# Kernel optimization log

Measured on AMD Instinct MI355X. Metric: run time of the kernel, lower is better.

Reference implementation:

```python
import jax, jax.numpy as jnp
import numpy as np

N_NODES = 100000
N_EDGES = 1600000
NFEAT = 256
NHID = 64
NHEADS = 8
NCLASS = 97
ALPHA = 0.2  # leaky relu slope
EPS = 1e-16  # guard against isolated rows (pyGAT divides by e_rowsum directly)


def _sp_gat_layer(x, Wk, ak, src, dst, n_nodes, alpha, concat):
    """One SpGraphAttentionLayer (eval mode, dropout off).
    x: [N, f_in], Wk: [f_in, f_out], ak: [2*f_out].
    edge e_ij = exp(-leakyrelu(a . [h_i || h_j])), out[i] = sum_j e_ij h_j / sum_j e_ij.
    """
    h = x @ Wk                          # [N, f_out]
    f_out = Wk.shape[1]
    s_src = h @ ak[:f_out]              # [N] = a1 . h_i
    s_dst = h @ ak[f_out:]              # [N] = a2 . h_j
    e = jnp.exp(-jax.nn.leaky_relu(s_src[src] + s_dst[dst], negative_slope=alpha))  # [E]
    rowsum = jax.ops.segment_sum(e, src, num_segments=n_nodes)                       # [N]
    num = jax.ops.segment_sum(e[:, None] * h[dst], src, num_segments=n_nodes)        # [N, f_out]
    h_prime = num / (rowsum[:, None] + EPS)
    return jax.nn.elu(h_prime) if concat else h_prime


def setup_inputs() -> dict:
    key = jax.random.key(0)
    ks = jax.random.split(key, 6)
    gain = 1.414  # xavier gain used by pyGAT
    features = jax.random.normal(ks[0], (N_NODES, NFEAT), dtype=jnp.float32)
    edge_index = jax.random.randint(ks[1], (2, N_EDGES), 0, N_NODES, dtype=jnp.int64)
    W = jax.random.normal(ks[2], (NHEADS, NFEAT, NHID), dtype=jnp.float32) * (gain * np.sqrt(2.0 / (NFEAT + NHID)))
    a = jax.random.normal(ks[3], (NHEADS, 2 * NHID), dtype=jnp.float32) * (gain * np.sqrt(2.0 / (1 + 2 * NHID)))
    W_out = jax.random.normal(ks[4], (NHEADS * NHID, NCLASS), dtype=jnp.float32) * (gain * np.sqrt(2.0 / (NHEADS * NHID + NCLASS)))
    a_out = jax.random.normal(ks[5], (2 * NCLASS,), dtype=jnp.float32) * (gain * np.sqrt(2.0 / (1 + 2 * NCLASS)))
    return {"features": features, "W": W, "a": a, "W_out": W_out, "a_out": a_out, "edge_index": edge_index}


def reference(features, W, a, W_out, a_out, edge_index):
    src, dst = edge_index[0], edge_index[1]
    n = features.shape[0]
    # multi-head hidden layer, concat heads (loop over small fixed head count to bound memory)
    heads = [
        _sp_gat_layer(features, W[k], a[k], src, dst, n, ALPHA, concat=True)
        for k in range(W.shape[0])
    ]
    x = jnp.concatenate(heads, axis=1)  # [N, nheads*nhid]
    # output attention layer (concat=False), then elu + log_softmax as in SpGAT.forward
    x = _sp_gat_layer(x, W_out, a_out, src, dst, n, ALPHA, concat=False)
    return jax.nn.log_softmax(jax.nn.elu(x), axis=1)
```

## Files before the change

kernel.cpp:

```cpp
#include <hip/hip_runtime.h>
#include <hip/hip_bf16.h>
#include <stdint.h>

typedef __attribute__((ext_vector_type(8))) short short8;
typedef __attribute__((ext_vector_type(4))) float floatx4;
typedef uint32_t u32;

#define N_NODES 100000
#define N_EDGES 1600000
#define ALPHA_SLOPE 0.2f
#define EPS_F 1e-16f

static __device__ __forceinline__ float bf2f(ushort h) {
    u32 u = ((u32)h) << 16;
    return __builtin_bit_cast(float, u);
}
static __device__ __forceinline__ ushort f2bf(float f) {
    u32 u = __builtin_bit_cast(u32, f);
    u32 r = (u + 0x7fffu + ((u >> 16) & 1u)) >> 16;
    return (ushort)r;
}
static __device__ __forceinline__ float edge_e(float s) {
    float lr = s > 0.f ? s : ALPHA_SLOPE * s;
    return __expf(-lr);
}

__global__ __launch_bounds__(256) void conv_feat(
    const float* __restrict__ in, ushort* __restrict__ out, int n4)
{
    int i = blockIdx.x * 256 + threadIdx.x;
    if (i < n4) {
        float4 v = ((const float4*)in)[i];
        ushort4 o;
        o.x = f2bf(v.x); o.y = f2bf(v.y); o.z = f2bf(v.z); o.w = f2bf(v.w);
        ((ushort4*)out)[i] = o;
    }
}

__global__ __launch_bounds__(256) void pretranspose(
    const float* __restrict__ W, const float* __restrict__ Wout,
    const float* __restrict__ a, const float* __restrict__ aout,
    ushort* __restrict__ Bp1, ushort* __restrict__ Bp2,
    float* __restrict__ acol1, float* __restrict__ acol2)
{
    int idx = blockIdx.x * 256 + threadIdx.x;
    if (idx < 256 * 512) {
        int k = idx >> 9, n = idx & 511;
        int head = n >> 6, c = n & 63;
        Bp1[((size_t)(k >> 3) * 512 + n) * 8 + (k & 7)] = f2bf(W[head * 16384 + k * 64 + c]);
    }
    if (idx < 512 * 128) {
        int k = idx >> 7, n = idx & 127;
        ushort v = (n < 97) ? f2bf(Wout[k * 97 + n]) : (ushort)0;
        Bp2[((size_t)(k >> 3) * 128 + n) * 8 + (k & 7)] = v;
    }
    if (idx < 512) {
        int head = idx >> 6, c = idx & 63;
        acol1[idx * 2]     = a[head * 128 + c];
        acol1[idx * 2 + 1] = a[head * 128 + 64 + c];
    }
    if (idx < 128) {
        acol2[idx * 2]     = (idx < 97) ? aout[idx] : 0.f;
        acol2[idx * 2 + 1] = (idx < 97) ? aout[97 + idx] : 0.f;
    }
}

__global__ __launch_bounds__(256) void gemm_mfma(
    const ushort* __restrict__ A, const ushort* __restrict__ Bp,
    ushort* __restrict__ C, const float* __restrict__ acol,
    float* __restrict__ ssrc_arr, float* __restrict__ sdst_arr,
    int sstride, int M, int K, int NP)
{
    __shared__ __align__(16) ushort Ald[4 * 128 * 8];
    const int tid = threadIdx.x;
    const int lane = tid & 63;
    const int wave = tid >> 6;
    const int wr = wave >> 1, wc = wave & 1;
    const int row0 = blockIdx.x * 128;
    const int col0 = blockIdx.y * 128;
    const int quad = lane >> 4;
    const int l16 = lane & 15;

    floatx4 acc[4][4] = {};

    for (int k0 = 0; k0 < K; k0 += 32) {
        __syncthreads();
#pragma unroll
        for (int i = 0; i < 2; ++i) {
            int q = i * 256 + tid;
            int r = q >> 2, kq = q & 3;
            int row = row0 + r;
            if (row >= M) row = M - 1;
            const uint4* src = (const uint4*)(A + (size_t)row * K + k0 + kq * 8);
            *(uint4*)(&Ald[((kq * 128 + r) * 8)]) = *src;
        }
        __syncthreads();

        short8 bfrag[4];
        int kqg = (k0 >> 3) + quad;
#pragma unroll
        for (int nt = 0; nt < 4; ++nt) {
            int col = col0 + wc * 64 + nt * 16 + l16;
            bfrag[nt] = *(const short8*)(Bp + ((size_t)kqg * NP + col) * 8);
        }
#pragma unroll
        for (int mt = 0; mt < 4; ++mt) {
            int r = wr * 64 + mt * 16 + l16;
            short8 afrag = *(const short8*)(&Ald[(quad * 128 + r) * 8]);
#pragma unroll
            for (int nt = 0; nt < 4; ++nt) {
                acc[mt][nt] = __builtin_amdgcn_mfma_f32_16x16x32_bf16(afrag, bfrag[nt], acc[mt][nt], 0, 0, 0);
            }
        }
    }

#pragma unroll
    for (int mt = 0; mt < 4; ++mt) {
#pragma unroll
        for (int rr = 0; rr < 4; ++rr) {
            int row = row0 + wr * 64 + mt * 16 + quad * 4 + rr;
            if (row < M) {
#pragma unroll
                for (int nt = 0; nt < 4; ++nt) {
                    int col = col0 + wc * 64 + nt * 16 + l16;
                    C[(size_t)row * NP + col] = f2bf(acc[mt][nt][rr]);
                }
            }
        }
    }

    float av1[4], av2[4];
#pragma unroll
    for (int nt = 0; nt < 4; ++nt) {
        int col = col0 + wc * 64 + nt * 16 + l16;
        av1[nt] = acol[col * 2];
        av2[nt] = acol[col * 2 + 1];
    }
    int g = (col0 + wc * 64) >> 6;
    int goff = (sstride > 1) ? g : 0;
#pragma unroll
    for (int mt = 0; mt < 4; ++mt) {
#pragma unroll
        for (int rr = 0; rr < 4; ++rr) {
            float p1 = 0.f, p2 = 0.f;
#pragma unroll
            for (int nt = 0; nt < 4; ++nt) {
                p1 = fmaf(acc[mt][nt][rr], av1[nt], p1);
                p2 = fmaf(acc[mt][nt][rr], av2[nt], p2);
            }
#pragma unroll
            for (int o = 1; o < 16; o <<= 1) {
                p1 += __shfl_xor(p1, o);
                p2 += __shfl_xor(p2, o);
            }
            int row = row0 + wr * 64 + mt * 16 + quad * 4 + rr;
            if (l16 == 0 && row < M) {
                atomicAdd(&ssrc_arr[(size_t)row * sstride + goff], p1);
                atomicAdd(&sdst_arr[(size_t)row * sstride + goff], p2);
            }
        }
    }
}

__global__ __launch_bounds__(256) void hist(const int* __restrict__ ei, int* __restrict__ cnt, int E) {
    int e = blockIdx.x * 256 + threadIdx.x;
    if (e < E) atomicAdd(&cnt[ei[e]], 1);
}

__global__ __launch_bounds__(256) void scan_partial(const int* __restrict__ cnt, int* __restrict__ bsum, int N) {
    int idx = blockIdx.x * 256 + threadIdx.x;
    int v = (idx < N) ? cnt[idx] : 0;
#pragma unroll
    for (int o = 32; o; o >>= 1) v += __shfl_xor(v, o);
    __shared__ int ws[4];
    if ((threadIdx.x & 63) == 0) ws[threadIdx.x >> 6] = v;
    __syncthreads();
    if (threadIdx.x == 0) bsum[blockIdx.x] = ws[0] + ws[1] + ws[2] + ws[3];
}

__global__ __launch_bounds__(512) void scan_block(int* __restrict__ bsum, int nb) {
    __shared__ int s[512];
    int t = threadIdx.x;
    int v = (t < nb) ? bsum[t] : 0;
    s[t] = v;
    __syncthreads();
    for (int o = 1; o < 512; o <<= 1) {
        int u = (t >= o) ? s[t - o] : 0;
        __syncthreads();
        s[t] += u;
        __syncthreads();
    }
    if (t < nb) bsum[t] = s[t] - v;
}

__global__ __launch_bounds__(256) void scan_final(
    const int* __restrict__ cnt, const int* __restrict__ bsum,
    int* __restrict__ row_ptr, int N, int E)
{
    int b = blockIdx.x, t = threadIdx.x;
    int idx = b * 256 + t;
    int v = (idx < N) ? cnt[idx] : 0;
    __shared__ int s[256];
    s[t] = v;
    __syncthreads();
    for (int o = 1; o < 256; o <<= 1) {
        int u = (t >= o) ? s[t - o] : 0;
        __syncthreads();
        s[t] += u;
        __syncthreads();
    }
    if (idx < N) row_ptr[idx] = bsum[b] + s[t] - v;
    if (idx == 0) row_ptr[N] = E;
}

__global__ __launch_bounds__(256) void fill_csr(
    const int* __restrict__ ei, const int* __restrict__ row_ptr,
    int* __restrict__ cur, int* __restrict__ col_idx, int* __restrict__ srow, int E)
{
    int e = blockIdx.x * 256 + threadIdx.x;
    if (e >= E) return;
    int s = ei[e];
    int d = ei[E + e];
    int p = atomicAdd(&cur[s], 1);
    int slot = row_ptr[s] + p;
    col_idx[slot] = d;
    srow[slot] = s;
}

__global__ __launch_bounds__(256) void ea1(
    const int* __restrict__ row_ptr, const int* __restrict__ col_idx,
    const ushort* __restrict__ h_all, const float* __restrict__ ssrc1,
    const float* __restrict__ sdst1, ushort* __restrict__ x1)
{
    int w = blockIdx.x * 4 + (threadIdx.x >> 6);
    int l = threadIdx.x & 63;
    int hl = l >> 3;
    int start = row_ptr[w], end = row_ptr[w + 1];
    float si = ssrc1[(size_t)w * 8 + hl];
    float acc[8] = {};
    float re = 0.f;
    int j = start;
    for (; j + 4 <= end; j += 4) {
        int d0 = col_idx[j], d1 = col_idx[j + 1], d2 = col_idx[j + 2], d3 = col_idx[j + 3];
        float e0 = edge_e(si + sdst1[(size_t)d0 * 8 + hl]);
        float e1 = edge_e(si + sdst1[(size_t)d1 * 8 + hl]);
        float e2 = edge_e(si + sdst1[(size_t)d2 * 8 + hl]);
        float e3 = edge_e(si + sdst1[(size_t)d3 * 8 + hl]);
        short8 v0 = *(const short8*)(h_all + (size_t)d0 * 512 + l * 8);
        short8 v1 = *(const short8*)(h_all + (size_t)d1 * 512 + l * 8);
        short8 v2 = *(const short8*)(h_all + (size_t)d2 * 512 + l * 8);
        short8 v3 = *(const short8*)(h_all + (size_t)d3 * 512 + l * 8);
        re += (e0 + e1) + (e2 + e3);
#pragma unroll
        for (int q = 0; q < 8; ++q) {
            float t0 = fmaf(e0, bf2f((ushort)v0[q]), e1 * bf2f((ushort)v1[q]));
            float t1 = fmaf(e2, bf2f((ushort)v2[q]), e3 * bf2f((ushort)v3[q]));
            acc[q] += t0 + t1;
        }
    }
    for (; j < end; ++j) {
        int d = col_idx[j];
        float e = edge_e(si + sdst1[(size_t)d * 8 + hl]);
        short8 hv = *(const short8*)(h_all + (size_t)d * 512 + l * 8);
        re += e;
#pragma unroll
        for (int q = 0; q < 8; ++q)
            acc[q] = fmaf(e, bf2f((ushort)hv[q]), acc[q]);
    }
    float inv = 1.f / (re + EPS_F);
    short8 o;
#pragma unroll
    for (int q = 0; q < 8; ++q) {
        float p = acc[q] * inv;
        p = p > 0.f ? p : expm1f(p);
        o[q] = (short)f2bf(p);
    }
    __builtin_nontemporal_store(o, (short8*)(x1 + (size_t)w * 512 + l * 8));
}

__global__ __launch_bounds__(256) void ea2(
    const int* __restrict__ row_ptr, const int* __restrict__ col_idx,
    const ushort* __restrict__ h2p, const float* __restrict__ s2src,
    const float* __restrict__ s2dst, float* __restrict__ out)
{
    int w = blockIdx.x * 4 + (threadIdx.x >> 6);
    int l = threadIdx.x & 63;
    int start = row_ptr[w], end = row_ptr[w + 1];
    float si = s2src[w];
    float a0 = 0.f, a1 = 0.f, re = 0.f;
    int j = start;
    for (; j + 4 <= end; j += 4) {
        int d0 = col_idx[j], d1 = col_idx[j + 1], d2 = col_idx[j + 2], d3 = col_idx[j + 3];
        float e0 = edge_e(si + s2dst[d0]);
        float e1 = edge_e(si + s2dst[d1]);
        float e2 = edge_e(si + s2dst[d2]);
        float e3 = edge_e(si + s2dst[d3]);
        u32 h0 = *(const u32*)(h2p + (size_t)d0 * 128 + 2 * l);
        u32 h1 = *(const u32*)(h2p + (size_t)d1 * 128 + 2 * l);
        u32 h2 = *(const u32*)(h2p + (size_t)d2 * 128 + 2 * l);
        u32 h3 = *(const u32*)(h2p + (size_t)d3 * 128 + 2 * l);
        re += (e0 + e1) + (e2 + e3);
        a0 += fmaf(e0, bf2f((ushort)(h0 & 0xffffu)), e1 * bf2f((ushort)(h1 & 0xffffu)))
            + fmaf(e2, bf2f((ushort)(h2 & 0xffffu)), e3 * bf2f((ushort)(h3 & 0xffffu)));
        a1 += fmaf(e0, bf2f((ushort)(h0 >> 16)), e1 * bf2f((ushort)(h1 >> 16)))
            + fmaf(e2, bf2f((ushort)(h2 >> 16)), e3 * bf2f((ushort)(h3 >> 16)));
    }
    for (; j < end; ++j) {
        int d = col_idx[j];
        float e = edge_e(si + s2dst[d]);
        u32 hv = *(const u32*)(h2p + (size_t)d * 128 + 2 * l);
        re += e;
        a0 = fmaf(e, bf2f((ushort)(hv & 0xffffu)), a0);
        a1 = fmaf(e, bf2f((ushort)(hv >> 16)), a1);
    }
    float inv = 1.f / (re + EPS_F);
    float v0 = a0 * inv, v1 = a1 * inv;
    v0 = v0 > 0.f ? v0 : expm1f(v0);
    v1 = v1 > 0.f ? v1 : expm1f(v1);
    int c0 = 2 * l, c1 = 2 * l + 1;
    bool val0 = c0 < 97, val1 = c1 < 97;
    float m = fmaxf(val0 ? v0 : -1e30f, val1 ? v1 : -1e30f);
#pragma unroll
    for (int o = 32; o; o >>= 1) m = fmaxf(m, __shfl_xor(m, o));
    float ex = (val0 ? __expf(v0 - m) : 0.f) + (val1 ? __expf(v1 - m) : 0.f);
#pragma unroll
    for (int o = 32; o; o >>= 1) ex += __shfl_xor(ex, o);
    float lt = m + logf(ex);
    if (val0) __builtin_nontemporal_store(v0 - lt, out + (size_t)w * 97 + c0);
    if (val1) __builtin_nontemporal_store(v1 - lt, out + (size_t)w * 97 + c1);
}

extern "C" void kernel_launch(void* const* d_in, const int* in_sizes, int n_in,
                              void* d_out, int out_size, void* d_ws, size_t ws_size,
                              hipStream_t stream)
{
    const float* feat = (const float*)d_in[0];
    const float* W    = (const float*)d_in[1];
    const float* a    = (const float*)d_in[2];
    const float* Wout = (const float*)d_in[3];
    const float* aout = (const float*)d_in[4];
    const int*   ei   = (const int*)d_in[5];
    float* out = (float*)d_out;

    const int N = N_NODES, E = N_EDGES;
    const int NB = (N + 255) / 256;

    char* base = (char*)d_ws;
    ushort* h_all = (ushort*)(base);
    ushort* x1    = (ushort*)(base + 102400000);
    ushort* featb = (ushort*)(base + 204800000);
    ushort* h2p   = (ushort*)(base + 204800000);
    char* tail = base + 256000000;
    float* ssrc1   = (float*)(tail + 0);
    float* sdst1   = (float*)(tail + 3200000);
    float* s2src   = (float*)(tail + 6400000);
    float* s2dst   = (float*)(tail + 6800000);
    int*   row_ptr = (int*)(tail + 7200000);
    int*   cnt     = (int*)(tail + 7600128);
    int*   col_idx = (int*)(tail + 8000128);
    int*   bsum    = (int*)(tail + 14400128);
    ushort* Bp1    = (ushort*)(tail + 14401920);
    ushort* Bp2    = (ushort*)(tail + 14664064);
    float* acol1   = (float*)(tail + 14795136);
    float* acol2   = (float*)(tail + 14799232);
    int*   srow    = (int*)(tail + 14800256);

    hipMemsetAsync(cnt, 0, (size_t)N * 4, stream);
    hipMemsetAsync(ssrc1, 0, (size_t)7200000, stream);
    conv_feat<<<(N * 256 / 4 + 255) / 256, 256, 0, stream>>>(feat, featb, N * 256 / 4);
    pretranspose<<<512, 256, 0, stream>>>(W, Wout, a, aout, Bp1, Bp2, acol1, acol2);

    gemm_mfma<<<dim3(782, 4), 256, 0, stream>>>(featb, Bp1, h_all, acol1, ssrc1, sdst1, 8, N, 256, 512);

    hist<<<(E + 255) / 256, 256, 0, stream>>>(ei, cnt, E);
    scan_partial<<<NB, 256, 0, stream>>>(cnt, bsum, N);
    scan_block<<<1, 512, 0, stream>>>(bsum, NB);
    scan_final<<<NB, 256, 0, stream>>>(cnt, bsum, row_ptr, N, E);
    hipMemsetAsync(cnt, 0, (size_t)N * 4, stream);
    fill_csr<<<(E + 255) / 256, 256, 0, stream>>>(ei, row_ptr, cnt, col_idx, srow, E);

    ea1<<<N / 4, 256, 0, stream>>>(row_ptr, col_idx, h_all, ssrc1, sdst1, x1);

    gemm_mfma<<<dim3(782, 1), 256, 0, stream>>>(x1, Bp2, h2p, acol2, s2src, s2dst, 1, N, 512, 128);
    ea2<<<N / 4, 256, 0, stream>>>(row_ptr, col_idx, h2p, s2src, s2dst, out);
}
```

Measured before the change: 865.5 us.

## Fuse prep kernels, deepen GEMM K-tile with swizzled LDS, narrow ea2 rows

Merges feature conversion, weight pre-transpose and the edge histogram into one prep kernel, and folds the memsets into a single contiguous clear with a separate cursor array. The GEMM now stages 64-wide K tiles into XOR-swizzled LDS and swaps grid axes so column blocks of the same row tile launch together. fill_csr stops writing the unused srow array, and ea2 handles a row with 32 lanes loading 4 bf16 values each. The aim is fewer launches, fewer LDS barriers and bank conflicts, and less wasted memory traffic. The risks are a larger LDS footprint and less parallelism per row in ea2.

```diff
diff --git a/kernel.cpp b/kernel.cpp
--- a/kernel.cpp
+++ b/kernel.cpp
@@ -25,43 +25,44 @@
     return __expf(-lr);
 }
 
-__global__ __launch_bounds__(256) void conv_feat(
-    const float* __restrict__ in, ushort* __restrict__ out, int n4)
-{
-    int i = blockIdx.x * 256 + threadIdx.x;
-    if (i < n4) {
-        float4 v = ((const float4*)in)[i];
+__global__ __launch_bounds__(256) void prep(
+    const float* __restrict__ feat, const float* __restrict__ W,
+    const float* __restrict__ Wout, const float* __restrict__ a,
+    const float* __restrict__ aout, const int* __restrict__ ei,
+    ushort* __restrict__ featb, ushort* __restrict__ Bp1, ushort* __restrict__ Bp2,
+    float* __restrict__ acol1, float* __restrict__ acol2, int* __restrict__ cnt)
+{
+    int b = blockIdx.x;
+    if (b < 25000) {
+        int i = b * 256 + threadIdx.x;
+        float4 v = ((const float4*)feat)[i];
         ushort4 o;
         o.x = f2bf(v.x); o.y = f2bf(v.y); o.z = f2bf(v.z); o.w = f2bf(v.w);
-        ((ushort4*)out)[i] = o;
-    }
-}
-
-__global__ __launch_bounds__(256) void pretranspose(
-    const float* __restrict__ W, const float* __restrict__ Wout,
-    const float* __restrict__ a, const float* __restrict__ aout,
-    ushort* __restrict__ Bp1, ushort* __restrict__ Bp2,
-    float* __restrict__ acol1, float* __restrict__ acol2)
-{
-    int idx = blockIdx.x * 256 + threadIdx.x;
-    if (idx < 256 * 512) {
-        int k = idx >> 9, n = idx & 511;
-        int head = n >> 6, c = n & 63;
-        Bp1[((size_t)(k >> 3) * 512 + n) * 8 + (k & 7)] = f2bf(W[head * 16384 + k * 64 + c]);
-    }
-    if (idx < 512 * 128) {
-        int k = idx >> 7, n = idx & 127;
-        ushort v = (n < 97) ? f2bf(Wout[k * 97 + n]) : (ushort)0;
-        Bp2[((size_t)(k >> 3) * 128 + n) * 8 + (k & 7)] = v;
-    }
-    if (idx < 512) {
-        int head = idx >> 6, c = idx & 63;
-        acol1[idx * 2]     = a[head * 128 + c];
-        acol1[idx * 2 + 1] = a[head * 128 + 64 + c];
-    }
-    if (idx < 128) {
-        acol2[idx * 2]     = (idx < 97) ? aout[idx] : 0.f;
-        acol2[idx * 2 + 1] = (idx < 97) ? aout[97 + idx] : 0.f;
+        ((ushort4*)featb)[i] = o;
+    } else if (b < 25512) {
+        int idx = (b - 25000) * 256 + threadIdx.x;
+        if (idx < 256 * 512) {
+            int k = idx >> 9, n = idx & 511;
+            int head = n >> 6, c = n & 63;
+            Bp1[((size_t)(k >> 3) * 512 + n) * 8 + (k & 7)] = f2bf(W[head * 16384 + k * 64 + c]);
+        }
+        if (idx < 512 * 128) {
+            int k = idx >> 7, n = idx & 127;
+            ushort v = (n < 97) ? f2bf(Wout[k * 97 + n]) : (ushort)0;
+            Bp2[((size_t)(k >> 3) * 128 + n) * 8 + (k & 7)] = v;
+        }
+        if (idx < 512) {
+            int head = idx >> 6, c = idx & 63;
+            acol1[idx * 2]     = a[head * 128 + c];
+            acol1[idx * 2 + 1] = a[head * 128 + 64 + c];
+        }
+        if (idx < 128) {
+            acol2[idx * 2]     = (idx < 97) ? aout[idx] : 0.f;
+            acol2[idx * 2 + 1] = (idx < 97) ? aout[97 + idx] : 0.f;
+        }
+    } else {
+        int e = (b - 25512) * 256 + threadIdx.x;
+        atomicAdd(&cnt[ei[e]], 1);
     }
 }
 
@@ -71,45 +72,49 @@
     float* __restrict__ ssrc_arr, float* __restrict__ sdst_arr,
     int sstride, int M, int K, int NP)
 {
-    __shared__ __align__(16) ushort Ald[4 * 128 * 8];
+    __shared__ __align__(16) ushort Ald[8 * 128 * 8];
     const int tid = threadIdx.x;
     const int lane = tid & 63;
     const int wave = tid >> 6;
     const int wr = wave >> 1, wc = wave & 1;
-    const int row0 = blockIdx.x * 128;
-    const int col0 = blockIdx.y * 128;
+    const int row0 = blockIdx.y * 128;
+    const int col0 = blockIdx.x * 128;
     const int quad = lane >> 4;
     const int l16 = lane & 15;
 
     floatx4 acc[4][4] = {};
 
-    for (int k0 = 0; k0 < K; k0 += 32) {
-        __syncthreads();
-#pragma unroll
-        for (int i = 0; i < 2; ++i) {
+    for (int k0 = 0; k0 < K; k0 += 64) {
+        __syncthreads();
+#pragma unroll
+        for (int i = 0; i < 4; ++i) {
             int q = i * 256 + tid;
-            int r = q >> 2, kq = q & 3;
+            int r = q >> 3, kq = q & 7;
             int row = row0 + r;
             if (row >= M) row = M - 1;
             const uint4* src = (const uint4*)(A + (size_t)row * K + k0 + kq * 8);
-            *(uint4*)(&Ald[((kq * 128 + r) * 8)]) = *src;
-        }
-        __syncthreads();
-
-        short8 bfrag[4];
-        int kqg = (k0 >> 3) + quad;
-#pragma unroll
-        for (int nt = 0; nt < 4; ++nt) {
-            int col = col0 + wc * 64 + nt * 16 + l16;
-            bfrag[nt] = *(const short8*)(Bp + ((size_t)kqg * NP + col) * 8);
-        }
-#pragma unroll
-        for (int mt = 0; mt < 4; ++mt) {
-            int r = wr * 64 + mt * 16 + l16;
-            short8 afrag = *(const short8*)(&Ald[(quad * 128 + r) * 8]);
+            *(uint4*)(&Ald[(kq * 128 + (r ^ kq)) * 8]) = *src;
+        }
+        __syncthreads();
+
+#pragma unroll
+        for (int s = 0; s < 2; ++s) {
+            int kqq = s * 4 + quad;
+            int kqg = (k0 >> 3) + kqq;
+            short8 bfrag[4];
 #pragma unroll
             for (int nt = 0; nt < 4; ++nt) {
-                acc[mt][nt] = __builtin_amdgcn_mfma_f32_16x16x32_bf16(afrag, bfrag[nt], acc[mt][nt], 0, 0, 0);
+                int col = col0 + wc * 64 + nt * 16 + l16;
+                bfrag[nt] = *(const short8*)(Bp + ((size_t)kqg * NP + col) * 8);
+            }
+#pragma unroll
+            for (int mt = 0; mt < 4; ++mt) {
+                int r = wr * 64 + mt * 16 + l16;
+                short8 afrag = *(const short8*)(&Ald[(kqq * 128 + (r ^ kqq)) * 8]);
+#pragma unroll
+                for (int nt = 0; nt < 4; ++nt) {
+                    acc[mt][nt] = __builtin_amdgcn_mfma_f32_16x16x32_bf16(afrag, bfrag[nt], acc[mt][nt], 0, 0, 0);
+                }
             }
         }
     }
@@ -160,11 +165,6 @@
             }
         }
     }
-}
-
-__global__ __launch_bounds__(256) void hist(const int* __restrict__ ei, int* __restrict__ cnt, int E) {
-    int e = blockIdx.x * 256 + threadIdx.x;
-    if (e < E) atomicAdd(&cnt[ei[e]], 1);
 }
 
 __global__ __launch_bounds__(256) void scan_partial(const int* __restrict__ cnt, int* __restrict__ bsum, int N) {
@@ -215,16 +215,14 @@
 
 __global__ __launch_bounds__(256) void fill_csr(
     const int* __restrict__ ei, const int* __restrict__ row_ptr,
-    int* __restrict__ cur, int* __restrict__ col_idx, int* __restrict__ srow, int E)
+    int* __restrict__ cur, int* __restrict__ col_idx, int E)
 {
     int e = blockIdx.x * 256 + threadIdx.x;
     if (e >= E) return;
     int s = ei[e];
     int d = ei[E + e];
     int p = atomicAdd(&cur[s], 1);
-    int slot = row_ptr[s] + p;
-    col_idx[slot] = d;
-    srow[slot] = s;
+    col_idx[row_ptr[s] + p] = d;
 }
 
 __global__ __launch_bounds__(256) void ea1(
@@ -283,11 +281,11 @@
     const ushort* __restrict__ h2p, const float* __restrict__ s2src,
     const float* __restrict__ s2dst, float* __restrict__ out)
 {
-    int w = blockIdx.x * 4 + (threadIdx.x >> 6);
-    int l = threadIdx.x & 63;
+    int w = blockIdx.x * 8 + (threadIdx.x >> 5);
+    int l = threadIdx.x & 31;
     int start = row_ptr[w], end = row_ptr[w + 1];
     float si = s2src[w];
-    float a0 = 0.f, a1 = 0.f, re = 0.f;
+    float a0 = 0.f, a1 = 0.f, a2 = 0.f, a3 = 0.f, re = 0.f;
     int j = start;
     for (; j + 4 <= end; j += 4) {
         int d0 = col_idx[j], d1 = col_idx[j + 1], d2 = col_idx[j + 2], d3 = col_idx[j + 3];
@@ -295,39 +293,47 @@
         float e1 = edge_e(si + s2dst[d1]);
         float e2 = edge_e(si + s2dst[d2]);
         float e3 = edge_e(si + s2dst[d3]);
-        u32 h0 = *(const u32*)(h2p + (size_t)d0 * 128 + 2 * l);
-        u32 h1 = *(const u32*)(h2p + (size_t)d1 * 128 + 2 * l);
-        u32 h2 = *(const u32*)(h2p + (size_t)d2 * 128 + 2 * l);
-        u32 h3 = *(const u32*)(h2p + (size_t)d3 * 128 + 2 * l);
+        ushort4 h0 = *(const ushort4*)(h2p + (size_t)d0 * 128 + 4 * l);
+        ushort4 h1 = *(const ushort4*)(h2p + (size_t)d1 * 128 + 4 * l);
+        ushort4 h2 = *(const ushort4*)(h2p + (size_t)d2 * 128 + 4 * l);
+        ushort4 h3 = *(const ushort4*)(h2p + (size_t)d3 * 128 + 4 * l);
         re += (e0 + e1) + (e2 + e3);
-        a0 += fmaf(e0, bf2f((ushort)(h0 & 0xffffu)), e1 * bf2f((ushort)(h1 & 0xffffu)))
-            + fmaf(e2, bf2f((ushort)(h2 & 0xffffu)), e3 * bf2f((ushort)(h3 & 0xffffu)));
-        a1 += fmaf(e0, bf2f((ushort)(h0 >> 16)), e1 * bf2f((ushort)(h1 >> 16)))
-            + fmaf(e2, bf2f((ushort)(h2 >> 16)), e3 * bf2f((ushort)(h3 >> 16)));
+        a0 += fmaf(e0, bf2f(h0.x), e1 * bf2f(h1.x)) + fmaf(e2, bf2f(h2.x), e3 * bf2f(h3.x));
+        a1 += fmaf(e0, bf2f(h0.y), e1 * bf2f(h1.y)) + fmaf(e2, bf2f(h2.y), e3 * bf2f(h3.y));
+        a2 += fmaf(e0, bf2f(h0.z), e1 * bf2f(h1.z)) + fmaf(e2, bf2f(h2.z), e3 * bf2f(h3.z));
+        a3 += fmaf(e0, bf2f(h0.w), e1 * bf2f(h1.w)) + fmaf(e2, bf2f(h2.w), e3 * bf2f(h3.w));
     }
     for (; j < end; ++j) {
         int d = col_idx[j];
         float e = edge_e(si + s2dst[d]);
-        u32 hv = *(const u32*)(h2p + (size_t)d * 128 + 2 * l);
+        ushort4 hv = *(const ushort4*)(h2p + (size_t)d * 128 + 4 * l);
         re += e;
-        a0 = fmaf(e, bf2f((ushort)(hv & 0xffffu)), a0);
-        a1 = fmaf(e, bf2f((ushort)(hv >> 16)), a1);
+        a0 = fmaf(e, bf2f(hv.x), a0);
+        a1 = fmaf(e, bf2f(hv.y), a1);
+        a2 = fmaf(e, bf2f(hv.z), a2);
+        a3 = fmaf(e, bf2f(hv.w), a3);
     }
     float inv = 1.f / (re + EPS_F);
-    float v0 = a0 * inv, v1 = a1 * inv;
-    v0 = v0 > 0.f ? v0 : expm1f(v0);
-    v1 = v1 > 0.f ? v1 : expm1f(v1);
-    int c0 = 2 * l, c1 = 2 * l + 1;
-    bool val0 = c0 < 97, val1 = c1 < 97;
-    float m = fmaxf(val0 ? v0 : -1e30f, val1 ? v1 : -1e30f);
-#pragma unroll
-    for (int o = 32; o; o >>= 1) m = fmaxf(m, __shfl_xor(m, o));
-    float ex = (val0 ? __expf(v0 - m) : 0.f) + (val1 ? __expf(v1 - m) : 0.f);
-#pragma unroll
-    for (int o = 32; o; o >>= 1) ex += __shfl_xor(ex, o);
+    float v[4] = { a0 * inv, a1 * inv, a2 * inv, a3 * inv };
+    bool val[4];
+    float m = -1e30f;
+#pragma unroll
+    for (int q = 0; q < 4; ++q) {
+        v[q] = v[q] > 0.f ? v[q] : expm1f(v[q]);
+        val[q] = (4 * l + q) < 97;
+        if (val[q]) m = fmaxf(m, v[q]);
+    }
+#pragma unroll
+    for (int o = 16; o; o >>= 1) m = fmaxf(m, __shfl_xor(m, o));
+    float ex = 0.f;
+#pragma unroll
+    for (int q = 0; q < 4; ++q) ex += val[q] ? __expf(v[q] - m) : 0.f;
+#pragma unroll
+    for (int o = 16; o; o >>= 1) ex += __shfl_xor(ex, o);
     float lt = m + logf(ex);
-    if (val0) __builtin_nontemporal_store(v0 - lt, out + (size_t)w * 97 + c0);
-    if (val1) __builtin_nontemporal_store(v1 - lt, out + (size_t)w * 97 + c1);
+#pragma unroll
+    for (int q = 0; q < 4; ++q)
+        if (val[q]) __builtin_nontemporal_store(v[q] - lt, out + (size_t)w * 97 + 4 * l + q);
 }
 
 extern "C" void kernel_launch(void* const* d_in, const int* in_sizes, int n_in,
@@ -357,30 +363,27 @@
     float* s2dst   = (float*)(tail + 6800000);
     int*   row_ptr = (int*)(tail + 7200000);
     int*   cnt     = (int*)(tail + 7600128);
-    int*   col_idx = (int*)(tail + 8000128);
-    int*   bsum    = (int*)(tail + 14400128);
-    ushort* Bp1    = (ushort*)(tail + 14401920);
-    ushort* Bp2    = (ushort*)(tail + 14664064);
-    float* acol1   = (float*)(tail + 14795136);
-    float* acol2   = (float*)(tail + 14799232);
-    int*   srow    = (int*)(tail + 14800256);
-
-    hipMemsetAsync(cnt, 0, (size_t)N * 4, stream);
-    hipMemsetAsync(ssrc1, 0, (size_t)7200000, stream);
-    conv_feat<<<(N * 256 / 4 + 255) / 256, 256, 0, stream>>>(feat, featb, N * 256 / 4);
-    pretranspose<<<512, 256, 0, stream>>>(W, Wout, a, aout, Bp1, Bp2, acol1, acol2);
-
-    gemm_mfma<<<dim3(782, 4), 256, 0, stream>>>(featb, Bp1, h_all, acol1, ssrc1, sdst1, 8, N, 256, 512);
-
-    hist<<<(E + 255) / 256, 256, 0, stream>>>(ei, cnt, E);
+    int*   cur     = (int*)(tail + 8000128);
+    int*   col_idx = (int*)(tail + 8400128);
+    int*   bsum    = (int*)(tail + 14800128);
+    ushort* Bp1    = (ushort*)(tail + 14801920);
+    ushort* Bp2    = (ushort*)(tail + 15064064);
+    float* acol1   = (float*)(tail + 15195136);
+    float* acol2   = (float*)(tail + 15199232);
+
+    hipMemsetAsync(ssrc1, 0, (size_t)8400128, stream);
+
+    prep<<<31762, 256, 0, stream>>>(feat, W, Wout, a, aout, ei, featb, Bp1, Bp2, acol1, acol2, cnt);
+
+    gemm_mfma<<<dim3(4, 782), 256, 0, stream>>>(featb, Bp1, h_all, acol1, ssrc1, sdst1, 8, N, 256, 512);
+
     scan_partial<<<NB, 256, 0, stream>>>(cnt, bsum, N);
     scan_block<<<1, 512, 0, stream>>>(bsum, NB);
     scan_final<<<NB, 256, 0, stream>>>(cnt, bsum, row_ptr, N, E);
-    hipMemsetAsync(cnt, 0, (size_t)N * 4, stream);
-    fill_csr<<<(E + 255) / 256, 256, 0, stream>>>(ei, row_ptr, cnt, col_idx, srow, E);
+    fill_csr<<<(E + 255) / 256, 256, 0, stream>>>(ei, row_ptr, cur, col_idx, E);
 
     ea1<<<N / 4, 256, 0, stream>>>(row_ptr, col_idx, h_all, ssrc1, sdst1, x1);
 
-    gemm_mfma<<<dim3(782, 1), 256, 0, stream>>>(x1, Bp2, h2p, acol2, s2src, s2dst, 1, N, 512, 128);
-    ea2<<<N / 4, 256, 0, stream>>>(row_ptr, col_idx, h2p, s2src, s2dst, out);
-}
+    gemm_mfma<<<dim3(1, 782), 256, 0, stream>>>(x1, Bp2, h2p, acol2, s2src, s2dst, 1, N, 512, 128);
+    ea2<<<N / 8, 256, 0, stream>>>(row_ptr, col_idx, h2p, s2src, s2dst, out);
+}
```

Result: faster. 825.2 us (-4.7%).
